# Optimization experiments

Hardware: AMD Instinct MI355X
Metric: run time of the kernel (lower is better)

## Reference

```python
import jax, jax.numpy as jnp
import numpy as np

B, T, C = 4, 2048, 1024
H, D = 16, 64


def setup_inputs() -> dict:
    key = jax.random.key(0)
    ks = jax.random.split(key, 6)
    s = 0.02
    return {
        "x": jax.random.normal(ks[0], (B, T, C), dtype=jnp.float32),
        "wq": jax.random.normal(ks[1], (H, C, D), dtype=jnp.float32) * s,
        "wk": jax.random.normal(ks[2], (H, C, D), dtype=jnp.float32) * s,
        "wv": jax.random.normal(ks[3], (H, C, D), dtype=jnp.float32) * s,
        "w_proj": jax.random.normal(ks[4], (C, C), dtype=jnp.float32) * s,
        "b_proj": jnp.zeros((C,), dtype=jnp.float32),
    }


def reference(x, wq, wk, wv, w_proj, b_proj):
    b, t, c = x.shape
    # per-head projections, vectorized over heads: [B,T,C] x [H,C,D] -> [B,H,T,D]
    q = jnp.einsum("btc,hcd->bhtd", x, wq)
    k = jnp.einsum("btc,hcd->bhtd", x, wk)
    v = jnp.einsum("btc,hcd->bhtd", x, wv)
    # NOTE: original scales by C**-0.5 where C = n_embd (not head_size)
    scale = jnp.asarray(c, x.dtype) ** -0.5
    scores = jnp.einsum("bhtd,bhsd->bhts", q, k) * scale  # [B,H,T,T]
    causal = jnp.tril(jnp.ones((t, t), dtype=bool))
    scores = jnp.where(causal, scores, jnp.finfo(x.dtype).min)
    wei = jax.nn.softmax(scores, axis=-1)
    out = jnp.einsum("bhts,bhsd->bhtd", wei, v)  # [B,H,T,D]
    out = out.transpose(0, 2, 1, 3).reshape(b, t, c)  # concat heads
    return out @ w_proj + b_proj
```

## Files before the change

### kernel.cpp

```cpp
#include <hip/hip_runtime.h>
#include <hip/hip_bf16.h>
#include <stdint.h>

#define B_ 4
#define T_ 2048
#define C_ 1024
#define H_ 16
#define D_ 64

typedef __attribute__((ext_vector_type(8))) short bf16x8;
typedef __attribute__((ext_vector_type(4))) short short4v;
typedef __attribute__((ext_vector_type(4))) float f32x4;

static __device__ __forceinline__ short f2bf(float f) {
    union { float f; unsigned u; } v; v.f = f;
    unsigned r = v.u + 0x7fffu + ((v.u >> 16) & 1u);
    return (short)(r >> 16);
}

static __device__ __forceinline__ float fast_exp2(float x) {
    float r;
    asm("v_exp_f32 %0, %1" : "=v"(r) : "v"(x));
    return r;
}

#define GLD_LDS16(g, l) __builtin_amdgcn_global_load_lds( \
    (const __attribute__((address_space(1))) void*)(g),   \
    (__attribute__((address_space(3))) void*)(l), 16, 0, 0)

#define QSCALE 0.04508422f

__global__ void pack_x(const float* __restrict__ x, short* __restrict__ xb) {
    int t = blockIdx.x * blockDim.x + threadIdx.x;
    const float* src = x + (size_t)t * 8;
    float4 v0 = *(const float4*)src;
    float4 v1 = *(const float4*)(src + 4);
    bf16x8 o;
    o[0] = f2bf(v0.x); o[1] = f2bf(v0.y); o[2] = f2bf(v0.z); o[3] = f2bf(v0.w);
    o[4] = f2bf(v1.x); o[5] = f2bf(v1.y); o[6] = f2bf(v1.z); o[7] = f2bf(v1.w);
    *(bf16x8*)(xb + (size_t)t * 8) = o;
}

__global__ void pack_wqkv2(const float* __restrict__ wq, const float* __restrict__ wk,
                           const float* __restrict__ wv, short* __restrict__ out) {
    __shared__ short tile[64][72];
    const int qh = blockIdx.y;
    const int qkv = qh >> 4, h = qh & 15;
    const int c0 = blockIdx.x * 64;
    const float* w = ((qkv == 0) ? wq : (qkv == 1) ? wk : wv) + (size_t)h * (C_ * D_);
    const int t = threadIdx.x;
    const int r = t >> 2;
    const int dc = (t & 3) * 16;

    const float* src = w + (size_t)(c0 + r) * D_ + dc;
#pragma unroll
    for (int j = 0; j < 4; ++j) {
        float4 v = *(const float4*)(src + j * 4);
        short4v s;
        s[0] = f2bf(v.x); s[1] = f2bf(v.y); s[2] = f2bf(v.z); s[3] = f2bf(v.w);
        *(short4v*)&tile[r][dc + j * 4] = s;
    }
    __syncthreads();

    const int d = t >> 2;
    const int cc = (t & 3) * 16;
    bf16x8 o0, o1;
#pragma unroll
    for (int j = 0; j < 8; ++j) {
        o0[j] = tile[cc + j][d];
        o1[j] = tile[cc + 8 + j][d];
    }
    short* dst = out + ((size_t)qkv * 1024 + h * 64 + d) * C_ + c0 + cc;
    *(bf16x8*)dst = o0;
    *(bf16x8*)(dst + 8) = o1;
}

__global__ void pack_wproj2(const float* __restrict__ wp, short* __restrict__ out) {
    __shared__ short tile[64][72];
    const int c0 = blockIdx.x * 64;
    const int n0 = blockIdx.y * 64;
    const int t = threadIdx.x;
    const int r = t >> 2;
    const int nc = (t & 3) * 16;

    const float* src = wp + (size_t)(c0 + r) * C_ + n0 + nc;
#pragma unroll
    for (int j = 0; j < 4; ++j) {
        float4 v = *(const float4*)(src + j * 4);
        short4v s;
        s[0] = f2bf(v.x); s[1] = f2bf(v.y); s[2] = f2bf(v.z); s[3] = f2bf(v.w);
        *(short4v*)&tile[r][nc + j * 4] = s;
    }
    __syncthreads();

    const int n = t >> 2;
    const int cc = (t & 3) * 16;
    bf16x8 o0, o1;
#pragma unroll
    for (int j = 0; j < 8; ++j) {
        o0[j] = tile[cc + j][n];
        o1[j] = tile[cc + 8 + j][n];
    }
    short* dst = out + (size_t)(n0 + n) * C_ + c0 + cc;
    *(bf16x8*)dst = o0;
    *(bf16x8*)(dst + 8) = o1;
}

template<int MODE>
__global__ __launch_bounds__(256)
void gemm_lds(const short* __restrict__ A, const short* __restrict__ Bt,
              void* __restrict__ Cptr, const float* __restrict__ bias,
              int M, int N, int K) {
    __shared__ short As[128 * 32];
    __shared__ short Bs[128 * 32];
    const int tid = threadIdx.x;
    const int lane = tid & 63, wid = tid >> 6;
    const int wr = wid >> 1, wc = wid & 1;
    const int l15 = lane & 15, l4 = lane >> 4;
    const int m0 = blockIdx.y * 128, n0 = blockIdx.x * 128;

    f32x4 acc[4][4] = {};

    for (int k0 = 0; k0 < K; k0 += 32) {
#pragma unroll
        for (int p = 0; p < 2; ++p) {
            int e = p * 256 + tid;
            int r = e >> 2, c = e & 3;
            GLD_LDS16(A  + (size_t)(m0 + r) * K + k0 + c * 8, As + e * 8);
            GLD_LDS16(Bt + (size_t)(n0 + r) * K + k0 + c * 8, Bs + e * 8);
        }
        __syncthreads();
        bf16x8 af[4], bfr[4];
#pragma unroll
        for (int m = 0; m < 4; ++m)
            af[m] = *(const bf16x8*)(As + (wr * 64 + m * 16 + l15) * 32 + l4 * 8);
#pragma unroll
        for (int n = 0; n < 4; ++n)
            bfr[n] = *(const bf16x8*)(Bs + (wc * 64 + n * 16 + l15) * 32 + l4 * 8);
#pragma unroll
        for (int m = 0; m < 4; ++m)
#pragma unroll
            for (int n = 0; n < 4; ++n)
                acc[m][n] = __builtin_amdgcn_mfma_f32_16x16x32_bf16(af[m], bfr[n], acc[m][n], 0, 0, 0);
        __syncthreads();
    }

#pragma unroll
    for (int m = 0; m < 4; ++m) {
        int row_base = m0 + wr * 64 + m * 16 + l4 * 4;
#pragma unroll
        for (int n = 0; n < 4; ++n) {
            int col = n0 + wc * 64 + n * 16 + l15;
#pragma unroll
            for (int r = 0; r < 4; ++r) {
                int row = row_base + r;
                float v = acc[m][n][r];
                if (MODE == 1) {
                    ((float*)Cptr)[(size_t)row * N + col] = v + bias[col];
                } else {
                    if (col < 1024) v *= QSCALE;
                    ((short*)Cptr)[(size_t)row * N + col] = f2bf(v);
                }
            }
        }
    }
}

__device__ __forceinline__ void softmax_pv_phase1(
    f32x4 S[4], f32x4 O[4], float* mrow, float* srow,
    int qrow0, int s0, bool diag, int l15, int l4, short* ps) {
    float pmax[4];
#pragma unroll
    for (int r = 0; r < 4; ++r) pmax[r] = -1e30f;
#pragma unroll
    for (int n = 0; n < 4; ++n) {
#pragma unroll
        for (int r = 0; r < 4; ++r) {
            float v = S[n][r];
            if (diag) {
                int scol = s0 + n * 16 + l15;
                if (scol > qrow0 + r) v = -1e30f;
            }
            S[n][r] = v;
            pmax[r] = fmaxf(pmax[r], v);
        }
    }
#pragma unroll
    for (int r = 0; r < 4; ++r) {
        float v = pmax[r];
        v = fmaxf(v, __shfl_xor(v, 1));
        v = fmaxf(v, __shfl_xor(v, 2));
        v = fmaxf(v, __shfl_xor(v, 4));
        v = fmaxf(v, __shfl_xor(v, 8));
        pmax[r] = v;
    }
    int ok = (pmax[0] <= mrow[0] + 8.0f) & (pmax[1] <= mrow[1] + 8.0f) &
             (pmax[2] <= mrow[2] + 8.0f) & (pmax[3] <= mrow[3] + 8.0f);
    if (!__all(ok)) {
#pragma unroll
        for (int r = 0; r < 4; ++r) {
            float mnew = fmaxf(mrow[r], pmax[r]);
            float fr = fast_exp2(mrow[r] - mnew);
            mrow[r] = mnew;
            srow[r] *= fr;
#pragma unroll
            for (int n = 0; n < 4; ++n) O[n][r] *= fr;
        }
    }
    float psum[4];
#pragma unroll
    for (int r = 0; r < 4; ++r) psum[r] = 0.0f;
#pragma unroll
    for (int n = 0; n < 4; ++n) {
#pragma unroll
        for (int r = 0; r < 4; ++r) {
            float p = fast_exp2(S[n][r] - mrow[r]);
            psum[r] += p;
            ps[(l4 * 4 + r) * 72 + n * 16 + l15] = f2bf(p);
        }
    }
#pragma unroll
    for (int r = 0; r < 4; ++r) {
        float v = psum[r];
        v += __shfl_xor(v, 1);
        v += __shfl_xor(v, 2);
        v += __shfl_xor(v, 4);
        v += __shfl_xor(v, 8);
        srow[r] += v;
    }
}

__global__ __launch_bounds__(256)
void attn_v13(const short* __restrict__ qkv, short* __restrict__ out) {
    const int pi = blockIdx.x;
    const int bh = blockIdx.y;
    const int b = bh >> 4;
    const int h = bh & 15;
    const int qA0 = pi * 64;
    const int qB0 = (31 - pi) * 64;
    const int ntA = pi + 1;
    const int ntB = 32 - pi;
    const int tid = threadIdx.x;
    const int wave = tid >> 6;
    const int lane = tid & 63;
    const int l15 = lane & 15, l4 = lane >> 4;

    __shared__ short Vt[64][72];
    __shared__ short Ps[4][2][16][72];

    const size_t rs = 3 * C_;
    const short* qbA = qkv + ((size_t)b * T_ + qA0) * rs + h * 64;
    const short* qbB = qkv + ((size_t)b * T_ + qB0) * rs + h * 64;
    const short* kb  = qkv + (size_t)b * T_ * rs + C_ + h * 64;
    const short* vb  = qkv + (size_t)b * T_ * rs + 2 * C_ + h * 64;

    bf16x8 aqA0 = *(const bf16x8*)(qbA + (size_t)(wave * 16 + l15) * rs + l4 * 8);
    bf16x8 aqA1 = *(const bf16x8*)(qbA + (size_t)(wave * 16 + l15) * rs + 32 + l4 * 8);
    bf16x8 aqB0 = *(const bf16x8*)(qbB + (size_t)(wave * 16 + l15) * rs + l4 * 8);
    bf16x8 aqB1 = *(const bf16x8*)(qbB + (size_t)(wave * 16 + l15) * rs + 32 + l4 * 8);

    f32x4 OA[4] = {}, OB[4] = {};
    float mA[4], sA[4], mB[4], sB[4];
#pragma unroll
    for (int r = 0; r < 4; ++r) { mA[r] = mB[r] = -1e30f; sA[r] = sB[r] = 0.0f; }

    short* psB = &Ps[wave][0][0][0];
    short* psA = &Ps[wave][1][0][0];

    for (int t = 0; t < ntB; ++t) {
        const int s0 = t * 64;
        const bool actA = (t < ntA);
        __syncthreads();

#pragma unroll
        for (int p = 0; p < 2; ++p) {
            int e = p * 256 + tid;
            int d = e & 63, sc = e >> 6;
            bf16x8 v;
#pragma unroll
            for (int j = 0; j < 8; ++j)
                v[j] = vb[(size_t)(s0 + sc * 8 + j) * rs + d];
            *(bf16x8*)&Vt[d][sc * 8] = v;
        }

        bf16x8 bk0[4], bk1[4];
#pragma unroll
        for (int n = 0; n < 4; ++n) {
            const short* kr = kb + (size_t)(s0 + n * 16 + l15) * rs;
            bk0[n] = *(const bf16x8*)(kr + l4 * 8);
            bk1[n] = *(const bf16x8*)(kr + 32 + l4 * 8);
        }

        f32x4 S[4];
#pragma unroll
        for (int n = 0; n < 4; ++n) {
            f32x4 z = {};
            z = __builtin_amdgcn_mfma_f32_16x16x32_bf16(aqB0, bk0[n], z, 0, 0, 0);
            S[n] = __builtin_amdgcn_mfma_f32_16x16x32_bf16(aqB1, bk1[n], z, 0, 0, 0);
        }
        softmax_pv_phase1(S, OB, mB, sB, qB0 + wave * 16 + l4 * 4, s0,
                          s0 == qB0, l15, l4, psB);

        if (actA) {
            f32x4 SA[4];
#pragma unroll
            for (int n = 0; n < 4; ++n) {
                f32x4 z = {};
                z = __builtin_amdgcn_mfma_f32_16x16x32_bf16(aqA0, bk0[n], z, 0, 0, 0);
                SA[n] = __builtin_amdgcn_mfma_f32_16x16x32_bf16(aqA1, bk1[n], z, 0, 0, 0);
            }
            softmax_pv_phase1(SA, OA, mA, sA, qA0 + wave * 16 + l4 * 4, s0,
                              s0 == qA0, l15, l4, psA);
        }

        __syncthreads();

        bf16x8 apB0 = *(const bf16x8*)(psB + l15 * 72 + l4 * 8);
        bf16x8 apB1 = *(const bf16x8*)(psB + l15 * 72 + 32 + l4 * 8);
#pragma unroll
        for (int n = 0; n < 4; ++n) {
            bf16x8 bv0 = *(const bf16x8*)&Vt[n * 16 + l15][l4 * 8];
            bf16x8 bv1 = *(const bf16x8*)&Vt[n * 16 + l15][32 + l4 * 8];
            OB[n] = __builtin_amdgcn_mfma_f32_16x16x32_bf16(apB0, bv0, OB[n], 0, 0, 0);
            OB[n] = __builtin_amdgcn_mfma_f32_16x16x32_bf16(apB1, bv1, OB[n], 0, 0, 0);
        }
        if (actA) {
            bf16x8 apA0 = *(const bf16x8*)(psA + l15 * 72 + l4 * 8);
            bf16x8 apA1 = *(const bf16x8*)(psA + l15 * 72 + 32 + l4 * 8);
#pragma unroll
            for (int n = 0; n < 4; ++n) {
                bf16x8 bv0 = *(const bf16x8*)&Vt[n * 16 + l15][l4 * 8];
                bf16x8 bv1 = *(const bf16x8*)&Vt[n * 16 + l15][32 + l4 * 8];
                OA[n] = __builtin_amdgcn_mfma_f32_16x16x32_bf16(apA0, bv0, OA[n], 0, 0, 0);
                OA[n] = __builtin_amdgcn_mfma_f32_16x16x32_bf16(apA1, bv1, OA[n], 0, 0, 0);
            }
        }
    }

#pragma unroll
    for (int r = 0; r < 4; ++r) {
        int rowB = qB0 + wave * 16 + l4 * 4 + r;
        int rowA = qA0 + wave * 16 + l4 * 4 + r;
        float invB = 1.0f / sB[r];
        float invA = 1.0f / sA[r];
        size_t obB = ((size_t)b * T_ + rowB) * C_ + h * 64;
        size_t obA = ((size_t)b * T_ + rowA) * C_ + h * 64;
#pragma unroll
        for (int n = 0; n < 4; ++n) {
            out[obB + n * 16 + l15] = f2bf(OB[n][r] * invB);
            out[obA + n * 16 + l15] = f2bf(OA[n][r] * invA);
        }
    }
}

extern "C" void kernel_launch(void* const* d_in, const int* in_sizes, int n_in,
                              void* d_out, int out_size, void* d_ws, size_t ws_size,
                              hipStream_t stream) {
    const float* x     = (const float*)d_in[0];
    const float* wq    = (const float*)d_in[1];
    const float* wk    = (const float*)d_in[2];
    const float* wv    = (const float*)d_in[3];
    const float* wproj = (const float*)d_in[4];
    const float* bproj = (const float*)d_in[5];
    float* out = (float*)d_out;

    short* wqkv_t  = (short*)d_ws;
    short* wproj_t = wqkv_t + 3072 * 1024;
    short* qkv_b   = wproj_t + 1024 * 1024;
    short* attn_b  = qkv_b + (size_t)8192 * 3072;
    short* xb      = attn_b;

    pack_x<<<4096, 256, 0, stream>>>(x, xb);
    pack_wqkv2<<<dim3(16, 48), 256, 0, stream>>>(wq, wk, wv, wqkv_t);
    pack_wproj2<<<dim3(16, 16), 256, 0, stream>>>(wproj, wproj_t);

    gemm_lds<2><<<dim3(24, 64), 256, 0, stream>>>(
        xb, wqkv_t, qkv_b, nullptr, 8192, 3072, 1024);

    attn_v13<<<dim3(16, 64), 256, 0, stream>>>(qkv_b, attn_b);

    gemm_lds<1><<<dim3(8, 64), 256, 0, stream>>>(
        attn_b, wproj_t, out, bproj, 8192, 1024, 1024);
}
```

Baseline: 297.0 us.

## Process two KV tiles per iteration with double-buffered V in attention

The attention loop now handles KV tiles in pairs. V for both tiles is transposed into a two-slot LDS buffer with one barrier pair, and the P·V matmul of the first tile is interleaved with the QK/softmax of the second. An odd trailing tile is handled in a separate tail. This halves the block-wide barriers per tile and gives the scheduler independent MFMA and softmax work to overlap, at the cost of more LDS and registers, which may lower occupancy.

```diff
diff --git a/kernel.cpp b/kernel.cpp
--- a/kernel.cpp
+++ b/kernel.cpp
@@ -166,7 +166,7 @@
     }
 }
 
-__device__ __forceinline__ void softmax_pv_phase1(
+__device__ __forceinline__ void softmax_phase(
     f32x4 S[4], f32x4 O[4], float* mrow, float* srow,
     int qrow0, int s0, bool diag, int l15, int l4, short* ps) {
     float pmax[4];
@@ -231,7 +231,7 @@
 }
 
 __global__ __launch_bounds__(256)
-void attn_v13(const short* __restrict__ qkv, short* __restrict__ out) {
+void attn_v14(const short* __restrict__ qkv, short* __restrict__ out) {
     const int pi = blockIdx.x;
     const int bh = blockIdx.y;
     const int b = bh >> 4;
@@ -245,7 +245,7 @@
     const int lane = tid & 63;
     const int l15 = lane & 15, l4 = lane >> 4;
 
-    __shared__ short Vt[64][72];
+    __shared__ short Vt[2][64][72];
     __shared__ short Ps[4][2][16][72];
 
     const size_t rs = 3 * C_;
@@ -266,23 +266,10 @@
 
     short* psB = &Ps[wave][0][0][0];
     short* psA = &Ps[wave][1][0][0];
-
-    for (int t = 0; t < ntB; ++t) {
-        const int s0 = t * 64;
-        const bool actA = (t < ntA);
-        __syncthreads();
-
-#pragma unroll
-        for (int p = 0; p < 2; ++p) {
-            int e = p * 256 + tid;
-            int d = e & 63, sc = e >> 6;
-            bf16x8 v;
-#pragma unroll
-            for (int j = 0; j < 8; ++j)
-                v[j] = vb[(size_t)(s0 + sc * 8 + j) * rs + d];
-            *(bf16x8*)&Vt[d][sc * 8] = v;
-        }
-
+    const int qrB = qB0 + wave * 16 + l4 * 4;
+    const int qrA = qA0 + wave * 16 + l4 * 4;
+
+    auto qk_sm = [&](int s0, bool actA) {
         bf16x8 bk0[4], bk1[4];
 #pragma unroll
         for (int n = 0; n < 4; ++n) {
@@ -290,7 +277,6 @@
             bk0[n] = *(const bf16x8*)(kr + l4 * 8);
             bk1[n] = *(const bf16x8*)(kr + 32 + l4 * 8);
         }
-
         f32x4 S[4];
 #pragma unroll
         for (int n = 0; n < 4; ++n) {
@@ -298,9 +284,7 @@
             z = __builtin_amdgcn_mfma_f32_16x16x32_bf16(aqB0, bk0[n], z, 0, 0, 0);
             S[n] = __builtin_amdgcn_mfma_f32_16x16x32_bf16(aqB1, bk1[n], z, 0, 0, 0);
         }
-        softmax_pv_phase1(S, OB, mB, sB, qB0 + wave * 16 + l4 * 4, s0,
-                          s0 == qB0, l15, l4, psB);
-
+        softmax_phase(S, OB, mB, sB, qrB, s0, s0 == qB0, l15, l4, psB);
         if (actA) {
             f32x4 SA[4];
 #pragma unroll
@@ -309,18 +293,17 @@
                 z = __builtin_amdgcn_mfma_f32_16x16x32_bf16(aqA0, bk0[n], z, 0, 0, 0);
                 SA[n] = __builtin_amdgcn_mfma_f32_16x16x32_bf16(aqA1, bk1[n], z, 0, 0, 0);
             }
-            softmax_pv_phase1(SA, OA, mA, sA, qA0 + wave * 16 + l4 * 4, s0,
-                              s0 == qA0, l15, l4, psA);
-        }
-
-        __syncthreads();
-
+            softmax_phase(SA, OA, mA, sA, qrA, s0, s0 == qA0, l15, l4, psA);
+        }
+    };
+
+    auto pv = [&](int slot, bool actA) {
         bf16x8 apB0 = *(const bf16x8*)(psB + l15 * 72 + l4 * 8);
         bf16x8 apB1 = *(const bf16x8*)(psB + l15 * 72 + 32 + l4 * 8);
 #pragma unroll
         for (int n = 0; n < 4; ++n) {
-            bf16x8 bv0 = *(const bf16x8*)&Vt[n * 16 + l15][l4 * 8];
-            bf16x8 bv1 = *(const bf16x8*)&Vt[n * 16 + l15][32 + l4 * 8];
+            bf16x8 bv0 = *(const bf16x8*)&Vt[slot][n * 16 + l15][l4 * 8];
+            bf16x8 bv1 = *(const bf16x8*)&Vt[slot][n * 16 + l15][32 + l4 * 8];
             OB[n] = __builtin_amdgcn_mfma_f32_16x16x32_bf16(apB0, bv0, OB[n], 0, 0, 0);
             OB[n] = __builtin_amdgcn_mfma_f32_16x16x32_bf16(apB1, bv1, OB[n], 0, 0, 0);
         }
@@ -329,12 +312,62 @@
             bf16x8 apA1 = *(const bf16x8*)(psA + l15 * 72 + 32 + l4 * 8);
 #pragma unroll
             for (int n = 0; n < 4; ++n) {
-                bf16x8 bv0 = *(const bf16x8*)&Vt[n * 16 + l15][l4 * 8];
-                bf16x8 bv1 = *(const bf16x8*)&Vt[n * 16 + l15][32 + l4 * 8];
+                bf16x8 bv0 = *(const bf16x8*)&Vt[slot][n * 16 + l15][l4 * 8];
+                bf16x8 bv1 = *(const bf16x8*)&Vt[slot][n * 16 + l15][32 + l4 * 8];
                 OA[n] = __builtin_amdgcn_mfma_f32_16x16x32_bf16(apA0, bv0, OA[n], 0, 0, 0);
                 OA[n] = __builtin_amdgcn_mfma_f32_16x16x32_bf16(apA1, bv1, OA[n], 0, 0, 0);
             }
         }
+    };
+
+    const int npair = ntB & ~1;
+    for (int t = 0; t < npair; t += 2) {
+        const int s0 = t * 64;
+        __syncthreads();
+
+#pragma unroll
+        for (int p = 0; p < 2; ++p) {
+            int e = p * 256 + tid;
+            int d = e & 63, sc = e >> 6;
+            bf16x8 v0, v1;
+#pragma unroll
+            for (int j = 0; j < 8; ++j) {
+                v0[j] = vb[(size_t)(s0 + sc * 8 + j) * rs + d];
+                v1[j] = vb[(size_t)(s0 + 64 + sc * 8 + j) * rs + d];
+            }
+            *(bf16x8*)&Vt[0][d][sc * 8] = v0;
+            *(bf16x8*)&Vt[1][d][sc * 8] = v1;
+        }
+
+        qk_sm(s0, t < ntA);
+
+        __syncthreads();
+
+        pv(0, t < ntA);
+        qk_sm(s0 + 64, t + 1 < ntA);
+
+        asm volatile("s_waitcnt lgkmcnt(0)" ::: "memory");
+        __builtin_amdgcn_sched_barrier(0);
+
+        pv(1, t + 1 < ntA);
+    }
+
+    if (ntB & 1) {
+        const int s0 = npair * 64;
+        __syncthreads();
+#pragma unroll
+        for (int p = 0; p < 2; ++p) {
+            int e = p * 256 + tid;
+            int d = e & 63, sc = e >> 6;
+            bf16x8 v0;
+#pragma unroll
+            for (int j = 0; j < 8; ++j)
+                v0[j] = vb[(size_t)(s0 + sc * 8 + j) * rs + d];
+            *(bf16x8*)&Vt[0][d][sc * 8] = v0;
+        }
+        qk_sm(s0, npair < ntA);
+        __syncthreads();
+        pv(0, npair < ntA);
     }
 
 #pragma unroll
@@ -377,7 +410,7 @@
     gemm_lds<2><<<dim3(24, 64), 256, 0, stream>>>(
         xb, wqkv_t, qkv_b, nullptr, 8192, 3072, 1024);
 
-    attn_v13<<<dim3(16, 64), 256, 0, stream>>>(qkv_b, attn_b);
+    attn_v14<<<dim3(16, 64), 256, 0, stream>>>(qkv_b, attn_b);
 
     gemm_lds<1><<<dim3(8, 64), 256, 0, stream>>>(
         attn_b, wproj_t, out, bproj, 8192, 1024, 1024);
```

New measurement: 288.7 us. -2.8%, faster.
